# Optimization experiments

Measured on AMD Instinct MI355X. Metric: run time of the kernel, lower is better.

Reference implementation:

```python
import jax, jax.numpy as jnp
import numpy as np

EPS_LN = 1e-12
EPS_BN = 1e-5


def layernorm(x, w, b):
    u = jnp.mean(x, axis=-1, keepdims=True)
    s = jnp.mean((x - u) ** 2, axis=-1, keepdims=True)
    return w * ((x - u) / jnp.sqrt(s + EPS_LN)) + b


def reps_block(x, ln1_w, ln1_b, lin_w, lin_b, ln2_w, ln2_b):
    # GRAPHLayerNorm -> (dropout, identity in eval) -> Linear -> ReLU -> GRAPHLayerNorm
    h = layernorm(x, ln1_w, ln1_b)
    h = jax.nn.relu(jnp.einsum('bnd,od->bno', h, lin_w) + lin_b)
    return layernorm(h, ln2_w, ln2_b)


def attend(x):
    # full dense self-attention: softmax(x x^T) x ; dropout is identity in eval
    scores = jnp.einsum('bnd,bmd->bnm', x, x)  # [B,4096,4096]
    attn = jax.nn.softmax(scores, axis=-1)
    return jnp.einsum('bnm,bmd->bnd', attn, x)


def setup_inputs() -> dict:
    key = jax.random.key(0)
    ks = jax.random.split(key, 8)
    B, C, H, W = 4, 512, 64, 64
    D = 512
    inp = {
        'T1': jax.random.normal(ks[0], (B, C, H, W), jnp.float32),
        'T2': jax.random.normal(ks[1], (B, C, H, W), jnp.float32),
        'w_conv3': jax.random.normal(ks[2], (1024, 1024, 3, 3), jnp.float32) * 0.01,
        'w_conv1': jax.random.normal(ks[3], (512, 1024, 1, 1), jnp.float32) * 0.03,
        'bn_gamma': jnp.ones((512,), jnp.float32),
        'bn_beta': jnp.zeros((512,), jnp.float32),
        'bn_mean': jnp.zeros((512,), jnp.float32),
        'bn_var': jnp.ones((512,), jnp.float32),
        'ln1_w': jnp.ones((D,), jnp.float32),
        'ln1_b': jnp.zeros((D,), jnp.float32),
        'lin_w': jax.random.normal(ks[4], (D, D), jnp.float32) * 0.04,
        'lin_b': jnp.zeros((D,), jnp.float32),
        'ln2_w': jnp.ones((D,), jnp.float32),
        'ln2_b': jnp.zeros((D,), jnp.float32),
    }
    return inp


def reference(T1, T2, w_conv3, w_conv1, bn_gamma, bn_beta, bn_mean, bn_var,
              ln1_w, ln1_b, lin_w, lin_b, ln2_w, ln2_b):
    B = T1.shape[0]
    X = jnp.concatenate((T1, T2), axis=1)  # [B,1024,64,64]
    dn = ('NCHW', 'OIHW', 'NCHW')
    X = jax.lax.conv_general_dilated(X, w_conv3, (1, 1), ((1, 1), (1, 1)), dimension_numbers=dn)
    X = jax.lax.conv_general_dilated(X, w_conv1, (1, 1), ((0, 0), (0, 0)), dimension_numbers=dn)  # [B,512,64,64]
    # BatchNorm (eval, running stats) + ReLU
    inv = (bn_gamma / jnp.sqrt(bn_var + EPS_BN))[None, :, None, None]
    X = jax.nn.relu(X * inv + (bn_beta - bn_mean * bn_gamma / jnp.sqrt(bn_var + EPS_BN))[None, :, None, None])
    x = X.transpose(0, 2, 3, 1).reshape(B, 4096, 512)
    # block 1
    rel = attend(x)
    rel = reps_block(x + rel, ln1_w, ln1_b, lin_w, lin_b, ln2_w, ln2_b)
    # block 2 (original code reuses self.reps_graph, i.e. SAME params)
    rel1 = attend(rel)
    rel1 = reps_block(rel + rel1, ln1_w, ln1_b, lin_w, lin_b, ln2_w, ln2_b)
    return rel1.reshape(B, 64, 64, 512).transpose(0, 3, 1, 2)  # [B,512,64,64]
```

## Files before the change

kernel.cpp:

```cpp
#include <hip/hip_runtime.h>
#include <stdint.h>

typedef float f32x4 __attribute__((ext_vector_type(4)));
typedef __bf16 bf16x8 __attribute__((ext_vector_type(8)));
typedef unsigned short u16;
typedef unsigned short u16x8 __attribute__((ext_vector_type(8)));

__device__ __forceinline__ float bf2f(u16 u){ unsigned int i = ((unsigned int)u)<<16; float f; __builtin_memcpy(&f,&i,4); return f; }
__device__ __forceinline__ u16 f2bf(float f){ unsigned int i; __builtin_memcpy(&i,&f,4); i += 0x7FFFu + ((i>>16)&1u); return (u16)(i>>16); }
__device__ __forceinline__ u16 f2h(float f){ _Float16 h = (_Float16)f; u16 b; __builtin_memcpy(&b,&h,2); return b; }
__device__ __forceinline__ float h2f(u16 b){ _Float16 h; __builtin_memcpy(&h,&b,2); return (float)h; }

__device__ __forceinline__ void gld16(const void* g, void* l){
  __builtin_amdgcn_global_load_lds(
      (const __attribute__((address_space(1))) void*)(uintptr_t)g,
      (__attribute__((address_space(3))) void*)(unsigned int)(uintptr_t)l, 16, 0, 0);
}

__global__ __launch_bounds__(256) void pad_interior(const float* __restrict__ T1,
                                                    const float* __restrict__ T2,
                                                    u16* __restrict__ Xpad){
  const int n = blockIdx.z, ct = blockIdx.y, pt = blockIdx.x;
  const int t = threadIdx.x;
  const int c0 = ct*64, p0 = pt*64;
  const float* src = (c0 < 512) ? (T1 + ((long)n*512 + c0)*4096)
                                : (T2 + ((long)n*512 + (c0-512))*4096);
  __shared__ u16 lds[64][66];
  #pragma unroll
  for (int i=0;i<4;i++){
    int c = i*16 + (t>>4);
    int ch = t&15;
    float4 v = *(const float4*)(src + (long)c*4096 + p0 + ch*4);
    int p = ch*4;
    lds[p+0][c] = f2bf(v.x); lds[p+1][c] = f2bf(v.y);
    lds[p+2][c] = f2bf(v.z); lds[p+3][c] = f2bf(v.w);
  }
  __syncthreads();
  #pragma unroll
  for (int i=0;i<8;i++){
    int p = i*8 + (t>>5);
    int c2 = t&31;
    int pix = p0 + p; int yy = (pix>>6)+1, xx = (pix&63)+1;
    ushort2 val; val.x = lds[p][2*c2]; val.y = lds[p][2*c2+1];
    *(ushort2*)(Xpad + (((long)n*66 + yy)*66 + xx)*1024 + c0 + 2*c2) = val;
  }
}

__global__ __launch_bounds__(256) void prep_w3(const float* __restrict__ w3, u16* __restrict__ wk3t){
  const int o = blockIdx.x; const int t = threadIdx.x;
  __shared__ u16 lds[9216];
  const float* src = w3 + (long)o*9216;
  #pragma unroll
  for (int i=0;i<9;i++){
    int j = i*256 + t;
    float4 v = *(const float4*)(src + j*4);
    lds[j*4+0]=f2bf(v.x); lds[j*4+1]=f2bf(v.y); lds[j*4+2]=f2bf(v.z); lds[j*4+3]=f2bf(v.w);
  }
  __syncthreads();
  u16* dst = wk3t + (long)o*9216;
  #pragma unroll
  for (int i=0;i<36;i++){
    int j = i*256 + t; int tp = j>>10, ci = j&1023;
    dst[j] = lds[ci*9+tp];
  }
}

__global__ void prep_small(const float* __restrict__ w1, const float* __restrict__ bg,
                           const float* __restrict__ bb, const float* __restrict__ bm,
                           const float* __restrict__ bv, const float* __restrict__ linw,
                           u16* __restrict__ w1t, u16* __restrict__ lint,
                           float* __restrict__ bias1){
  const int b = blockIdx.x, t = threadIdx.x;
  if (b < 2048){
    long i = (long)b*256 + t;
    int o = (int)(i>>10);
    float inv = bg[o] / sqrtf(bv[o] + 1e-5f);
    w1t[i] = f2bf(w1[i]*inv);
  } else if (b < 3072){
    long i = (long)(b-2048)*256 + t;
    lint[i] = f2bf(linw[i]);
  } else {
    int o = (b-3072)*256 + t;
    float inv = bg[o]/sqrtf(bv[o]+1e-5f);
    bias1[o] = bb[o] - bm[o]*inv;
  }
}

__global__ __launch_bounds__(256) void row_norm(const u16* __restrict__ x, float* __restrict__ nrm){
  const int row = blockIdx.x*4 + (threadIdx.x>>6);
  const int lane = threadIdx.x & 63;
  u16x8 q = *(const u16x8*)(x + (long)row*512 + lane*8);
  float s = 0.f;
  #pragma unroll
  for (int j=0;j<8;j++){ float f = bf2f(q[j]); s += f*f; }
  #pragma unroll
  for (int off=32; off; off>>=1) s += __shfl_xor(s, off);
  if (lane==0) nrm[row] = s;
}

__global__ __launch_bounds__(256) void transpose_bf(const u16* __restrict__ src, u16* __restrict__ dst,
                                                    int R, int C, long sStr, long dStr){
  const int z = blockIdx.z;
  src += (long)z*sStr; dst += (long)z*dStr;
  const int r0 = blockIdx.x*64, c0 = blockIdx.y*64;
  const int t = threadIdx.x;
  __shared__ u16 lds[64][66];
  #pragma unroll
  for (int i=0;i<4;i++){
    int r = i*16 + (t>>4), ch = t&15;
    ushort4 v = *(const ushort4*)(src + (long)(r0+r)*C + c0 + ch*4);
    lds[r][ch*4+0]=v.x; lds[r][ch*4+1]=v.y; lds[r][ch*4+2]=v.z; lds[r][ch*4+3]=v.w;
  }
  __syncthreads();
  #pragma unroll
  for (int i=0;i<4;i++){
    int c = i*16 + (t>>4), ch = t&15;
    ushort4 v;
    v.x = lds[ch*4+0][c]; v.y = lds[ch*4+1][c]; v.z = lds[ch*4+2][c]; v.w = lds[ch*4+3][c];
    *(ushort4*)(dst + (long)(c0+c)*R + r0 + ch*4) = v;
  }
}

__global__ __launch_bounds__(256) void transpose_bf_f32(const u16* __restrict__ src, float* __restrict__ dst){
  const int z = blockIdx.z;
  src += (long)z*4096*512; dst += (long)z*512*4096;
  const int r0 = blockIdx.x*64, c0 = blockIdx.y*64;
  const int t = threadIdx.x;
  __shared__ u16 lds[64][66];
  #pragma unroll
  for (int i=0;i<4;i++){
    int r = i*16 + (t>>4), ch = t&15;
    ushort4 v = *(const ushort4*)(src + (long)(r0+r)*512 + c0 + ch*4);
    lds[r][ch*4+0]=v.x; lds[r][ch*4+1]=v.y; lds[r][ch*4+2]=v.z; lds[r][ch*4+3]=v.w;
  }
  __syncthreads();
  #pragma unroll
  for (int i=0;i<4;i++){
    int c = i*16 + (t>>4), ch = t&15;
    float4 v;
    v.x = bf2f(lds[ch*4+0][c]); v.y = bf2f(lds[ch*4+1][c]);
    v.z = bf2f(lds[ch*4+2][c]); v.w = bf2f(lds[ch*4+3][c]);
    *(float4*)(dst + (long)(c0+c)*4096 + r0 + ch*4) = v;
  }
}

template<int EPI, int CONV>
__global__ __launch_bounds__(512, 2) void gemm256(
    const u16* __restrict__ Ain, const u16* __restrict__ Btin, void* __restrict__ Cv,
    int K, int lda, int ldb, int ldc, const float* __restrict__ srowIn,
    u16* __restrict__ C0, u16* __restrict__ C1, u16* __restrict__ C2, u16* __restrict__ C3)
{
  extern __shared__ u16 sm[];
  const int t = threadIdx.x;
  const int lane = t & 63;
  const int wid = t >> 6;
  const int wr = wid >> 2, wc = wid & 3;

  const int orig = blockIdx.y * gridDim.x + blockIdx.x;
  const int cpx = (gridDim.x * gridDim.y) >> 3;
  const int swz = (orig & 7) * cpx + (orig >> 3);
  const int bx = swz % gridDim.x;
  const int by = swz / gridDim.x;
  const long m0 = (long)by * 256, n0 = (long)bx * 256;

  const u16* A = Ain;
  const u16* Bt = Btin;
  const float* srow = srowIn;
  u16* Cz = (u16*)Cv;
  if (EPI == 3){
    const int z = blockIdx.z;
    A = Ain + (long)z*4096*lda;
    Bt = A;
    srow = srowIn + (long)z*4096;
    Cz = (z==0)?C0:(z==1)?C1:(z==2)?C2:C3;
  }

  const int row0 = t >> 2;
  const int cs0  = (t & 3) ^ ((row0 >> 1) & 3);

  const u16 *aB0, *aB1;
  if (CONV) {
    long m_ = m0 + row0;
    long pb0 = ((long)((int)(m_>>12)*66 + (int)((m_>>6)&63)))*66 + (int)(m_&63);
    m_ = m0 + row0 + 128;
    long pb1 = ((long)((int)(m_>>12)*66 + (int)((m_>>6)&63)))*66 + (int)(m_&63);
    aB0 = A + pb0*1024 + cs0*8;
    aB1 = A + pb1*1024 + cs0*8;
  } else {
    aB0 = A + (m0 + row0)*(long)lda + cs0*8;
    aB1 = A + (m0 + row0 + 128)*(long)lda + cs0*8;
  }
  const u16* bB0 = Bt + (n0 + row0)*(long)ldb + cs0*8;
  const u16* bB1 = Bt + (n0 + row0 + 128)*(long)ldb + cs0*8;

  auto issueA = [&](int sub, long aoff){
    u16* d = sm + sub*8192 + t*8;
    gld16(aB0 + aoff, d);
    gld16(aB1 + aoff, d + 4096);
  };
  auto issueB = [&](int sub, long boff){
    u16* d = sm + 32768 + sub*8192 + t*8;
    gld16(bB0 + boff, d);
    gld16(bB1 + boff, d + 4096);
  };
  auto conv_aoff = [&](int tile)->long {
    int kb = tile << 6;
    int tap = kb >> 10;
    int cb  = kb & 1023;
    int ky = (tap >= 6) ? 2 : (tap >= 3 ? 1 : 0);
    int kx = tap - ky*3;
    return (long)(ky*66 + kx)*1024 + cb;
  };

  const int frow = lane & 15;
  const int elemoff = (((lane>>4) ^ ((frow>>1)&3)) << 3);
  const int rAoff = (wr*128 + frow)*32 + elemoff;
  const int rBoff = (wc*64  + frow)*32 + elemoff;

  f32x4 acc[8][4] = {};

  {
    long a0 = CONV ? conv_aoff(0) : 0L;
    issueA(0, a0);
    issueB(0, 0);
    issueA(1, a0 + 32);
    issueB(1, 32);
  }

  const int NT = K >> 6;
  for (int tile = 0; tile < NT; ++tile) {
    const int b = tile & 1;
    const int nb2 = b ^ 1;
    const bool lastT = (tile == NT-1);
    long aoffN = 0, boffN = 0;
    if (!lastT) {
      aoffN = CONV ? conv_aoff(tile+1) : (long)(tile+1)*64;
      boffN = (long)(tile+1)*64;
    }

    asm volatile("s_waitcnt vmcnt(4)" ::: "memory");
    __builtin_amdgcn_s_barrier();
    __builtin_amdgcn_sched_barrier(0);

    {
      const u16* pA = sm + (b*2+0)*8192 + rAoff;
      const u16* pB = sm + 32768 + (b*2+0)*8192 + rBoff;
      bf16x8 bf[4];
      #pragma unroll
      for (int i=0;i<4;i++) bf[i] = *(const bf16x8*)(pB + i*512);
      {
        bf16x8 a[4];
        #pragma unroll
        for (int i=0;i<4;i++) a[i] = *(const bf16x8*)(pA + i*512);
        if (!lastT) issueA(nb2*2+0, aoffN);
        __builtin_amdgcn_s_setprio(1);
        #pragma unroll
        for (int mi=0;mi<4;mi++)
          #pragma unroll
          for (int ni=0;ni<4;ni++)
            acc[mi][ni] = __builtin_amdgcn_mfma_f32_16x16x32_bf16(a[mi], bf[ni], acc[mi][ni],0,0,0);
        __builtin_amdgcn_s_setprio(0);
      }
      {
        bf16x8 a[4];
        #pragma unroll
        for (int i=0;i<4;i++) a[i] = *(const bf16x8*)(pA + (4+i)*512);
        if (!lastT) issueB(nb2*2+0, boffN);
        __builtin_amdgcn_s_setprio(1);
        #pragma unroll
        for (int mi=0;mi<4;mi++)
          #pragma unroll
          for (int ni=0;ni<4;ni++)
            acc[4+mi][ni] = __builtin_amdgcn_mfma_f32_16x16x32_bf16(a[mi], bf[ni], acc[4+mi][ni],0,0,0);
        __builtin_amdgcn_s_setprio(0);
      }
    }

    if (lastT) asm volatile("s_waitcnt vmcnt(0)" ::: "memory");
    else       asm volatile("s_waitcnt vmcnt(4)" ::: "memory");
    __builtin_amdgcn_s_barrier();
    __builtin_amdgcn_sched_barrier(0);

    {
      const u16* pA = sm + (b*2+1)*8192 + rAoff;
      const u16* pB = sm + 32768 + (b*2+1)*8192 + rBoff;
      bf16x8 bf[4];
      #pragma unroll
      for (int i=0;i<4;i++) bf[i] = *(const bf16x8*)(pB + i*512);
      {
        bf16x8 a[4];
        #pragma unroll
        for (int i=0;i<4;i++) a[i] = *(const bf16x8*)(pA + i*512);
        if (!lastT) issueA(nb2*2+1, aoffN + 32);
        __builtin_amdgcn_s_setprio(1);
        #pragma unroll
        for (int mi=0;mi<4;mi++)
          #pragma unroll
          for (int ni=0;ni<4;ni++)
            acc[mi][ni] = __builtin_amdgcn_mfma_f32_16x16x32_bf16(a[mi], bf[ni], acc[mi][ni],0,0,0);
        __builtin_amdgcn_s_setprio(0);
      }
      {
        bf16x8 a[4];
        #pragma unroll
        for (int i=0;i<4;i++) a[i] = *(const bf16x8*)(pA + (4+i)*512);
        if (!lastT) issueB(nb2*2+1, boffN + 32);
        __builtin_amdgcn_s_setprio(1);
        #pragma unroll
        for (int mi=0;mi<4;mi++)
          #pragma unroll
          for (int ni=0;ni<4;ni++)
            acc[4+mi][ni] = __builtin_amdgcn_mfma_f32_16x16x32_bf16(a[mi], bf[ni], acc[4+mi][ni],0,0,0);
        __builtin_amdgcn_s_setprio(0);
      }
    }
  }

  const int crow0 = wr*128 + ((lane>>4)<<2);
  const int ccol0 = wc*64 + frow;
  #pragma unroll
  for (int mi=0;mi<8;mi++){
    #pragma unroll
    for (int ni=0;ni<4;ni++){
      long col = n0 + ccol0 + ni*16;
      #pragma unroll
      for (int r=0;r<4;r++){
        long row = m0 + crow0 + mi*16 + r;
        float v = acc[mi][ni][r];
        if (EPI==3) Cz[row*(long)ldc + col] = f2h(v - srow[row]);
        else        Cz[row*(long)ldc + col] = f2bf(v);
      }
    }
  }
}

template<int EPI>
__global__ __launch_bounds__(256, 2) void gemm_bt(
    const u16* __restrict__ A, const u16* __restrict__ Bt,
    void* __restrict__ Cv, const float* __restrict__ bias,
    int K, int lda, int ldb, int ldc)
{
  const int t = threadIdx.x;
  const int lane = t & 63;
  const int w = t >> 6;
  const int wr = w >> 1, wc = w & 1;
  const long m0 = (long)blockIdx.y * 128;
  const long n0 = (long)blockIdx.x * 128;

  __shared__ u16 lA[128*32];
  __shared__ u16 lB[128*32];

  const u16* aS0 = A + (m0 + (t>>2))*(long)lda + (t&3)*8;
  const u16* aS1 = aS0 + 64*(long)lda;
  const u16* bS0 = Bt + (n0 + (t>>2))*(long)ldb + (t&3)*8;
  const u16* bS1 = bS0 + 64*(long)ldb;
  u16* dA0 = lA + t*8; u16* dA1 = lA + 2048 + t*8;
  u16* dB0 = lB + t*8; u16* dB1 = lB + 2048 + t*8;

  f32x4 acc[4][4] = {};
  const int frow = lane & 15, kq = (lane >> 4) * 8;
  const u16* rA = lA + (wr*64 + frow)*32 + kq;
  const u16* rB = lB + (wc*64 + frow)*32 + kq;

  for (int kb = 0; kb < K; kb += 32) {
    gld16(aS0 + kb, dA0); gld16(aS1 + kb, dA1);
    gld16(bS0 + kb, dB0); gld16(bS1 + kb, dB1);
    __syncthreads();
    bf16x8 af[4], bfr[4];
    #pragma unroll
    for (int i=0;i<4;i++) af[i]  = *(const bf16x8*)(rA + i*512);
    #pragma unroll
    for (int i=0;i<4;i++) bfr[i] = *(const bf16x8*)(rB + i*512);
    #pragma unroll
    for (int mi=0;mi<4;mi++)
      #pragma unroll
      for (int ni=0;ni<4;ni++)
        acc[mi][ni] = __builtin_amdgcn_mfma_f32_16x16x32_bf16(af[mi], bfr[ni], acc[mi][ni], 0,0,0);
    __syncthreads();
  }

  const int crow0 = wr*64 + ((lane>>4)<<2);
  const int ccol0 = wc*64 + (lane&15);
  #pragma unroll
  for (int mi=0;mi<4;mi++){
    #pragma unroll
    for (int ni=0;ni<4;ni++){
      long col = n0 + ccol0 + ni*16;
      float bv = (EPI==1) ? bias[col] : 0.0f;
      #pragma unroll
      for (int r=0;r<4;r++){
        long row = m0 + crow0 + mi*16 + r;
        float v = acc[mi][ni][r];
        if (EPI==1){ v += bv; v = v > 0.0f ? v : 0.0f; }
        ((u16*)Cv)[row*(long)ldc + col] = f2bf(v);
      }
    }
  }
}

__global__ __launch_bounds__(256, 2) void pv5(
    const u16* __restrict__ P0, const u16* __restrict__ P1,
    const u16* __restrict__ P2, const u16* __restrict__ P3,
    const u16* __restrict__ xT, u16* __restrict__ attb)
{
  extern __shared__ u16 pm[];
  const int L = blockIdx.x;
  const int xcd = L & 7;
  const int z = xcd >> 1;
  const int tile = ((L >> 3) << 1) + (xcd & 1);
  const int bx = tile & 3, by = tile >> 2;
  const long ZS = 4096L*512;
  const u16* A  = (z==0)?P0:(z==1)?P1:(z==2)?P2:P3;
  const u16* Bt = xT   + (long)z*ZS;
  u16*       C  = attb + (long)z*ZS;
  const long m0 = (long)by * 128, n0 = (long)bx * 128;

  const int t = threadIdx.x;
  const int lane = t & 63;
  const int w = t >> 6;
  const int wr = w >> 1, wc = w & 1;

  const int row0 = t >> 2;
  const int cs0  = (t & 3) ^ ((row0 >> 1) & 3);

  const u16* aB0 = A + (m0 + row0)*4096L + cs0*8;
  const u16* aB1 = aB0 + 64*4096L;
  const u16* bB0 = Bt + (n0 + row0)*4096L + cs0*8;
  const u16* bB1 = bB0 + 64*4096L;

  auto issueA = [&](int sub, long off){
    u16* d = pm + sub*4096 + t*8;
    gld16(aB0 + off, d);
    gld16(aB1 + off, d + 2048);
  };
  auto issueB = [&](int sub, long off){
    u16* d = pm + 16384 + sub*4096 + t*8;
    gld16(bB0 + off, d);
    gld16(bB1 + off, d + 2048);
  };

  const int frow = lane & 15;
  const int elemoff = (((lane>>4) ^ ((frow>>1)&3)) << 3);
  const int rAoff = (wr*64 + frow)*32 + elemoff;
  const int rBoff = (wc*64 + frow)*32 + elemoff;

  f32x4 acc[4][4] = {};

  issueA(0, 0);  issueB(0, 0);
  issueA(1, 32); issueB(1, 32);

  const int NT = 64;
  for (int tl = 0; tl < NT; ++tl) {
    const int b = tl & 1;
    const int nb2 = b ^ 1;
    const bool lastT = (tl == NT-1);
    const long offN = (long)(tl+1)*64;

    asm volatile("s_waitcnt vmcnt(4)" ::: "memory");
    __builtin_amdgcn_s_barrier();
    __builtin_amdgcn_sched_barrier(0);

    {
      const u16* pA = pm + (b*2+0)*4096 + rAoff;
      const u16* pB = pm + 16384 + (b*2+0)*4096 + rBoff;
      bf16x8 bf[4];
      #pragma unroll
      for (int i=0;i<4;i++) bf[i] = *(const bf16x8*)(pB + i*512);
      {
        bf16x8 a[2];
        #pragma unroll
        for (int i=0;i<2;i++) a[i] = *(const bf16x8*)(pA + i*512);
        if (!lastT) issueA(nb2*2+0, offN);
        __builtin_amdgcn_s_setprio(1);
        #pragma unroll
        for (int mi=0;mi<2;mi++)
          #pragma unroll
          for (int ni=0;ni<4;ni++)
            acc[mi][ni] = __builtin_amdgcn_mfma_f32_16x16x32_bf16(a[mi], bf[ni], acc[mi][ni],0,0,0);
        __builtin_amdgcn_s_setprio(0);
      }
      {
        bf16x8 a[2];
        #pragma unroll
        for (int i=0;i<2;i++) a[i] = *(const bf16x8*)(pA + (2+i)*512);
        if (!lastT) issueB(nb2*2+0, offN);
        __builtin_amdgcn_s_setprio(1);
        #pragma unroll
        for (int mi=0;mi<2;mi++)
          #pragma unroll
          for (int ni=0;ni<4;ni++)
            acc[2+mi][ni] = __builtin_amdgcn_mfma_f32_16x16x32_bf16(a[mi], bf[ni], acc[2+mi][ni],0,0,0);
        __builtin_amdgcn_s_setprio(0);
      }
    }

    if (lastT) asm volatile("s_waitcnt vmcnt(0)" ::: "memory");
    else       asm volatile("s_waitcnt vmcnt(4)" ::: "memory");
    __builtin_amdgcn_s_barrier();
    __builtin_amdgcn_sched_barrier(0);

    {
      const u16* pA = pm + (b*2+1)*4096 + rAoff;
      const u16* pB = pm + 16384 + (b*2+1)*4096 + rBoff;
      bf16x8 bf[4];
      #pragma unroll
      for (int i=0;i<4;i++) bf[i] = *(const bf16x8*)(pB + i*512);
      {
        bf16x8 a[2];
        #pragma unroll
        for (int i=0;i<2;i++) a[i] = *(const bf16x8*)(pA + i*512);
        if (!lastT) issueA(nb2*2+1, offN + 32);
        __builtin_amdgcn_s_setprio(1);
        #pragma unroll
        for (int mi=0;mi<2;mi++)
          #pragma unroll
          for (int ni=0;ni<4;ni++)
            acc[mi][ni] = __builtin_amdgcn_mfma_f32_16x16x32_bf16(a[mi], bf[ni], acc[mi][ni],0,0,0);
        __builtin_amdgcn_s_setprio(0);
      }
      {
        bf16x8 a[2];
        #pragma unroll
        for (int i=0;i<2;i++) a[i] = *(const bf16x8*)(pA + (2+i)*512);
        if (!lastT) issueB(nb2*2+1, offN + 32);
        __builtin_amdgcn_s_setprio(1);
        #pragma unroll
        for (int mi=0;mi<2;mi++)
          #pragma unroll
          for (int ni=0;ni<4;ni++)
            acc[2+mi][ni] = __builtin_amdgcn_mfma_f32_16x16x32_bf16(a[mi], bf[ni], acc[2+mi][ni],0,0,0);
        __builtin_amdgcn_s_setprio(0);
      }
    }
  }

  const int crow0 = wr*64 + ((lane>>4)<<2);
  const int ccol0 = wc*64 + frow;
  #pragma unroll
  for (int mi=0;mi<4;mi++){
    #pragma unroll
    for (int ni=0;ni<4;ni++){
      long col = n0 + ccol0 + ni*16;
      #pragma unroll
      for (int r=0;r<4;r++){
        long row = m0 + crow0 + mi*16 + r;
        C[row*512 + col] = f2bf(acc[mi][ni][r]);
      }
    }
  }
}

__global__ __launch_bounds__(256) void softmax_batched(
    u16* __restrict__ S0, u16* __restrict__ S1,
    u16* __restrict__ S2, u16* __restrict__ S3)
{
  const int z = blockIdx.x >> 12;
  const long row = blockIdx.x & 4095;
  u16* buf = (z==0)?S0:(z==1)?S1:(z==2)?S2:S3;
  u16* src = buf + row*4096;
  const int t = threadIdx.x, lane = t&63, w = t>>6;
  float v[16];
  #pragma unroll
  for (int i=0;i<2;i++){
    u16x8 q = *(const u16x8*)(src + t*16 + i*8);
    #pragma unroll
    for (int j=0;j<8;j++) v[i*8+j] = h2f(q[j]);
  }
  float mx = v[0];
  #pragma unroll
  for (int i=1;i<16;i++) mx = fmaxf(mx, v[i]);
  #pragma unroll
  for (int off=32; off; off>>=1) mx = fmaxf(mx, __shfl_xor(mx, off));
  __shared__ float red[4];
  if (lane==0) red[w] = mx;
  __syncthreads();
  mx = fmaxf(fmaxf(red[0],red[1]), fmaxf(red[2],red[3]));
  float sum = 0.0f;
  #pragma unroll
  for (int i=0;i<16;i++){ v[i] = __expf(v[i]-mx); sum += v[i]; }
  #pragma unroll
  for (int off=32; off; off>>=1) sum += __shfl_xor(sum, off);
  __shared__ float red2[4];
  if (lane==0) red2[w] = sum;
  __syncthreads();
  sum = red2[0]+red2[1]+red2[2]+red2[3];
  const float inv = 1.0f/sum;
  #pragma unroll
  for (int i=0;i<2;i++){
    u16x8 o;
    #pragma unroll
    for (int j=0;j<8;j++) o[j] = f2bf(v[i*8+j]*inv);
    *(u16x8*)(src + t*16 + i*8) = o;
  }
}

template<int ADD>
__global__ __launch_bounds__(256) void ln_row(
    const u16* __restrict__ X, const u16* __restrict__ Y,
    const float* __restrict__ w, const float* __restrict__ b,
    u16* __restrict__ outB)
{
  const long row = blockIdx.x;
  const int t = threadIdx.x, lane = t&63, wv = t>>6;
  ushort2 xv = *(const ushort2*)(X + row*512 + t*2);
  float v0 = bf2f(xv.x), v1 = bf2f(xv.y);
  if (ADD){
    ushort2 yv = *(const ushort2*)(Y + row*512 + t*2);
    v0 += bf2f(yv.x); v1 += bf2f(yv.y);
  }
  float s = v0+v1, q = v0*v0 + v1*v1;
  #pragma unroll
  for (int off=32; off; off>>=1){ s += __shfl_xor(s,off); q += __shfl_xor(q,off); }
  __shared__ float red[8];
  if (lane==0){ red[wv]=s; red[4+wv]=q; }
  __syncthreads();
  s = red[0]+red[1]+red[2]+red[3];
  q = red[4]+red[5]+red[6]+red[7];
  const float u = s*(1.0f/512.0f);
  const float var = q*(1.0f/512.0f) - u*u;
  const float inv = rsqrtf(var + 1e-12f);
  const int c = t*2;
  float o0 = (v0-u)*inv*w[c]   + b[c];
  float o1 = (v1-u)*inv*w[c+1] + b[c+1];
  ushort2 ov; ov.x=f2bf(o0); ov.y=f2bf(o1);
  *(ushort2*)(outB + row*512 + c) = ov;
}

extern "C" void kernel_launch(void* const* d_in, const int* in_sizes, int n_in,
                              void* d_out, int out_size, void* d_ws, size_t ws_size,
                              hipStream_t stream) {
  const float* T1   = (const float*)d_in[0];
  const float* T2   = (const float*)d_in[1];
  const float* w3   = (const float*)d_in[2];
  const float* w1   = (const float*)d_in[3];
  const float* bg   = (const float*)d_in[4];
  const float* bb   = (const float*)d_in[5];
  const float* bm   = (const float*)d_in[6];
  const float* bv   = (const float*)d_in[7];
  const float* ln1w = (const float*)d_in[8];
  const float* ln1b = (const float*)d_in[9];
  const float* linw = (const float*)d_in[10];
  const float* linb = (const float*)d_in[11];
  const float* ln2w = (const float*)d_in[12];
  const float* ln2b = (const float*)d_in[13];

  hipFuncSetAttribute(reinterpret_cast<const void*>(gemm256<0,1>),
                      hipFuncAttributeMaxDynamicSharedMemorySize, 131072);
  hipFuncSetAttribute(reinterpret_cast<const void*>(gemm256<3,0>),
                      hipFuncAttributeMaxDynamicSharedMemorySize, 131072);
  hipFuncSetAttribute(reinterpret_cast<const void*>(pv5),
                      hipFuncAttributeMaxDynamicSharedMemorySize, 65536);

  char* ws = (char*)d_ws;
  size_t off = 0;
  auto alloc = [&](size_t bytes)->char* {
    char* p = ws + off;
    off += (bytes + 255) & ~(size_t)255;
    return p;
  };
  const size_t XPAD_B = 4L*66*66*1024*2;
  u16*   Xpad  = (u16*)  alloc(XPAD_B);
  u16*   wk3t  = (u16*)  alloc(1024L*9216*2);
  u16*   w1t   = (u16*)  alloc(512L*1024*2);
  u16*   lint  = (u16*)  alloc(512L*512*2);
  float* bias1 = (float*)alloc(512*4);
  float* nrm   = (float*)alloc(16384L*4);
  u16*   Y1    = (u16*)  alloc(16384L*1024*2);
  u16*   x0    = (u16*)  alloc(16384L*512*2);
  u16*   xT    = (u16*)  alloc(4L*512*4096*2);
  u16*   Sreg  = (u16*)  alloc(2L*4096*4096*2);
  u16*   attb  = (u16*)  alloc(16384L*512*2);
  u16*   h     = (u16*)  alloc(16384L*512*2);
  u16*   g     = (u16*)  alloc(16384L*512*2);
  u16*   rel1  = (u16*)  alloc(16384L*512*2);
  u16*   S0    = Y1;
  u16*   S1    = Sreg;
  u16*   S2    = Sreg + 4096L*4096;
  u16*   S3    = Xpad;
  if (off > ws_size) return;

  const long ZS = 4096L*512;

  hipMemsetAsync(Xpad, 0, XPAD_B, stream);
  pad_interior<<<dim3(64,16,4), 256, 0, stream>>>(T1, T2, Xpad);
  prep_w3<<<1024, 256, 0, stream>>>(w3, wk3t);
  prep_small<<<3074, 256, 0, stream>>>(w1, bg, bb, bm, bv, linw, w1t, lint, bias1);

  gemm256<0,1><<<dim3(4,64), 512, 131072, stream>>>(Xpad, wk3t, (void*)Y1, 9216, 0, 9216, 1024,
                                                    nullptr, nullptr, nullptr, nullptr, nullptr);
  gemm_bt<1><<<dim3(4,128), 256, 0, stream>>>(Y1, w1t, (void*)x0, bias1, 1024, 1024, 1024, 512);

  auto attend = [&](const u16* xin){
    transpose_bf<<<dim3(64,8,4), 256, 0, stream>>>(xin, xT, 4096, 512, ZS, ZS);
    row_norm<<<4096, 256, 0, stream>>>(xin, nrm);
    gemm256<3,0><<<dim3(16,16,4), 512, 131072, stream>>>(xin, xin, nullptr, 512, 512, 512, 4096,
                                                         nrm, S0, S1, S2, S3);
    softmax_batched<<<16384, 256, 0, stream>>>(S0, S1, S2, S3);
    pv5<<<512, 256, 65536, stream>>>(S0, S1, S2, S3, xT, attb);
  };

  attend(x0);
  ln_row<1><<<16384, 256, 0, stream>>>(x0, attb, ln1w, ln1b, h);
  gemm_bt<1><<<dim3(4,128), 256, 0, stream>>>(h, lint, (void*)g, linb, 512, 512, 512, 512);
  ln_row<0><<<16384, 256, 0, stream>>>(g, nullptr, ln2w, ln2b, rel1);

  attend(rel1);
  ln_row<1><<<16384, 256, 0, stream>>>(rel1, attb, ln1w, ln1b, h);
  gemm_bt<1><<<dim3(4,128), 256, 0, stream>>>(h, lint, (void*)g, linb, 512, 512, 512, 512);
  ln_row<0><<<16384, 256, 0, stream>>>(g, nullptr, ln2w, ln2b, x0);

  transpose_bf_f32<<<dim3(64,8,4), 256, 0, stream>>>(x0, (float*)d_out);
}
```

Before: 856.0 us.

## Exploit symmetry of x·xᵀ scores by computing only upper-triangular tiles

```diff
diff --git a/kernel.cpp b/kernel.cpp
--- a/kernel.cpp
+++ b/kernel.cpp
@@ -156,23 +156,31 @@
   const int wid = t >> 6;
   const int wr = wid >> 2, wc = wid & 3;
 
-  const int orig = blockIdx.y * gridDim.x + blockIdx.x;
-  const int cpx = (gridDim.x * gridDim.y) >> 3;
-  const int swz = (orig & 7) * cpx + (orig >> 3);
-  const int bx = swz % gridDim.x;
-  const int by = swz / gridDim.x;
-  const long m0 = (long)by * 256, n0 = (long)bx * 256;
-
-  const u16* A = Ain;
-  const u16* Bt = Btin;
-  const float* srow = srowIn;
-  u16* Cz = (u16*)Cv;
+  long m0, n0;
+  int byv = 0, bxv = 0;
+  const u16* A; const u16* Bt; const float* srow; u16* Cz;
   if (EPI == 3){
-    const int z = blockIdx.z;
+    const int orig = blockIdx.x;
+    const int swz = (orig & 7) * 68 + (orig >> 3);
+    const int z = swz / 136;
+    int p = swz % 136;
+    int by = 0;
+    while (p >= 16 - by){ p -= 16 - by; by++; }
+    const int bx = by + p;
+    byv = by; bxv = bx;
+    m0 = (long)by * 256; n0 = (long)bx * 256;
     A = Ain + (long)z*4096*lda;
     Bt = A;
     srow = srowIn + (long)z*4096;
     Cz = (z==0)?C0:(z==1)?C1:(z==2)?C2:C3;
+  } else {
+    const int orig = blockIdx.y * gridDim.x + blockIdx.x;
+    const int cpx = (gridDim.x * gridDim.y) >> 3;
+    const int swz = (orig & 7) * cpx + (orig >> 3);
+    const int bx = swz % gridDim.x;
+    const int by = swz / gridDim.x;
+    m0 = (long)by * 256; n0 = (long)bx * 256;
+    A = Ain; Bt = Btin; srow = srowIn; Cz = (u16*)Cv;
   }
 
   const int row0 = t >> 2;
@@ -318,6 +326,7 @@
 
   const int crow0 = wr*128 + ((lane>>4)<<2);
   const int ccol0 = wc*64 + frow;
+
   #pragma unroll
   for (int mi=0;mi<8;mi++){
     #pragma unroll
@@ -330,6 +339,39 @@
         if (EPI==3) Cz[row*(long)ldc + col] = f2h(v - srow[row]);
         else        Cz[row*(long)ldc + col] = f2bf(v);
       }
+    }
+  }
+
+  if (EPI == 3 && bxv != byv){
+    __syncthreads();
+    u16* lt = sm;
+    float sc[4];
+    #pragma unroll
+    for (int ni=0;ni<4;ni++) sc[ni] = srow[n0 + ccol0 + ni*16];
+    #pragma unroll
+    for (int mi=0;mi<8;mi++){
+      const int g = (crow0 + mi*16) >> 2;
+      #pragma unroll
+      for (int ni=0;ni<4;ni++){
+        const int col_l = ccol0 + ni*16;
+        ushort4 pk;
+        #pragma unroll
+        for (int r=0;r<4;r++) pk[r] = f2h(acc[mi][ni][r] - sc[ni]);
+        *(ushort4*)(lt + col_l*256 + ((g ^ (col_l & 63))<<2)) = pk;
+      }
+    }
+    __syncthreads();
+    const int half = lane >> 5, l32 = lane & 31;
+    #pragma unroll
+    for (int ps=0; ps<16; ps++){
+      const int R = ps*16 + wid*2 + half;
+      const int u0 = ((l32<<1)    ) ^ (R & 63);
+      const int u1 = ((l32<<1) | 1) ^ (R & 63);
+      ushort4 a = *(const ushort4*)(lt + R*256 + (u0<<2));
+      ushort4 b = *(const ushort4*)(lt + R*256 + (u1<<2));
+      u16* dst = Cz + (n0 + R)*(long)ldc + m0 + (l32<<3);
+      *(ushort4*)dst = a;
+      *(ushort4*)(dst+4) = b;
     }
   }
 }
@@ -693,8 +735,8 @@
   auto attend = [&](const u16* xin){
     transpose_bf<<<dim3(64,8,4), 256, 0, stream>>>(xin, xT, 4096, 512, ZS, ZS);
     row_norm<<<4096, 256, 0, stream>>>(xin, nrm);
-    gemm256<3,0><<<dim3(16,16,4), 512, 131072, stream>>>(xin, xin, nullptr, 512, 512, 512, 4096,
-                                                         nrm, S0, S1, S2, S3);
+    gemm256<3,0><<<dim3(544), 512, 131072, stream>>>(xin, xin, nullptr, 512, 512, 512, 4096,
+                                                     nrm, S0, S1, S2, S3);
     softmax_batched<<<16384, 256, 0, stream>>>(S0, S1, S2, S3);
     pv5<<<512, 256, 65536, stream>>>(S0, S1, S2, S3, xT, attb);
   };
```

New measurement: 814.5 us. -4.9%, faster.
